# Kernel optimization log

Hardware: AMD Instinct MI355X
Metric: run time of the kernel (lower is better)

## Reference

```python
import jax, jax.numpy as jnp
import numpy as np

EMB = 1024
HEADS = 16
S = EMB // HEADS  # per-head dim


def setup_inputs() -> dict:
    key = jax.random.key(0)
    ks = jax.random.split(key, 6)
    x = jax.random.normal(ks[0], (4, 2048, EMB), dtype=jnp.float32)
    # torch nn.Linear(s, s, bias=False): weight [out, in], y = x @ W.T
    Wk = jax.random.normal(ks[1], (S, S), dtype=jnp.float32) * (1.0 / np.sqrt(S))
    Wq = jax.random.normal(ks[2], (S, S), dtype=jnp.float32) * (1.0 / np.sqrt(S))
    Wv = jax.random.normal(ks[3], (S, S), dtype=jnp.float32) * (1.0 / np.sqrt(S))
    # unifyHeads: Linear(heads*s, emb) with bias
    Wu = jax.random.normal(ks[4], (EMB, EMB), dtype=jnp.float32) * (1.0 / np.sqrt(EMB))
    bu = jax.random.normal(ks[5], (EMB,), dtype=jnp.float32) * 0.01
    return {"x": x, "Wk": Wk, "Wq": Wq, "Wv": Wv, "Wu": Wu, "bu": bu}


def reference(x, Wk, Wq, Wv, Wu, bu):
    b, t, e = x.shape
    h, s = HEADS, S
    x4 = x.reshape(b, t, h, s)
    # per-head narrow projections (y = x @ W.T)
    k = jnp.einsum('bths,os->bhto', x4, Wk)  # [b,h,t,s]
    q = jnp.einsum('bths,os->bhto', x4, Wq)
    v = jnp.einsum('bths,os->bhto', x4, Wv)
    scale = e ** 0.25
    q = q / scale
    k = k / scale
    dot = jnp.einsum('bhqs,bhks->bhqk', q, k)  # [b,h,t,t]
    attn = jax.nn.softmax(dot, axis=-1)
    out = jnp.einsum('bhqk,bhks->bhqs', attn, v)  # [b,h,t,s]
    out = out.transpose(0, 2, 1, 3).reshape(b, t, h * s)
    return out @ Wu.T + bu
```

## Files before the change

kernel.cpp:

```cpp
#include <hip/hip_runtime.h>
#include <hip/hip_bf16.h>

#define BB 4
#define TT 2048
#define HH 16
#define SS 64
#define EE 1024

typedef __attribute__((ext_vector_type(8))) short short8;
typedef __attribute__((ext_vector_type(4))) short short4v;
typedef __attribute__((ext_vector_type(4))) float float4v;
typedef unsigned long long ull;

__device__ inline short f2bf(float f) {
    union { __hip_bfloat16 h; short s; } u;
    u.h = __float2bfloat16(f);
    return u.s;
}

__device__ inline unsigned pack_bf(float lo, float hi) {
    return ((unsigned)(unsigned short)f2bf(hi) << 16) | (unsigned short)f2bf(lo);
}

__device__ inline unsigned pack_trunc(float lo, float hi) {
    unsigned a = __builtin_bit_cast(unsigned, lo);
    unsigned b = __builtin_bit_cast(unsigned, hi);
    return (b & 0xFFFF0000u) | (a >> 16);
}

__device__ inline float4v mfma16(short8 a, short8 b, float4v c) {
    return __builtin_amdgcn_mfma_f32_16x16x32_bf16(a, b, c, 0, 0, 0);
}

#define LDSP(p) ((__attribute__((address_space(3))) void*)(p))
#define GLBP(p) ((const __attribute__((address_space(1))) void*)(p))

__global__ __launch_bounds__(256) void k_qkv(
    const float* __restrict__ x, const float* __restrict__ Wk,
    const float* __restrict__ Wq, const float* __restrict__ Wv,
    short* __restrict__ qb, short* __restrict__ kb, short* __restrict__ vb)
{
    __shared__ __attribute__((aligned(16))) short lw[3][64][72];
    const int tid = threadIdx.x;
    const float sq = 0.21233045f;

    for (int i = 0; i < 12; i++) {
        int u = tid + 256 * i;
        int w = u >> 10;
        int rem = u & 1023;
        int row = rem >> 4;
        int col = (rem & 15) * 4;
        const float* Wp = (w == 0) ? Wk : ((w == 1) ? Wq : Wv);
        float4v f = *reinterpret_cast<const float4v*>(Wp + row * 64 + col);
        float sc = (w == 2) ? 1.0f : sq;
        short4v s4;
        s4.x = f2bf(f.x * sc); s4.y = f2bf(f.y * sc);
        s4.z = f2bf(f.z * sc); s4.w = f2bf(f.w * sc);
        *reinterpret_cast<short4v*>(&lw[w][row][col]) = s4;
    }
    __syncthreads();

    const int wave = tid >> 6, lane = tid & 63;
    const int quad = lane >> 4, m = lane & 15;
    const long r0 = (long)blockIdx.x * 64 + wave * 16;
    const int bt = (int)(r0 >> 4);
    const int b = bt >> 11, t = bt & 2047;

    const float* xrow = x + (r0 + m) * 64;
    short8 af[2];
    for (int ks = 0; ks < 2; ks++) {
        float4v f0 = *reinterpret_cast<const float4v*>(xrow + ks * 32 + quad * 8);
        float4v f1 = *reinterpret_cast<const float4v*>(xrow + ks * 32 + quad * 8 + 4);
        short8 a;
        a[0] = f2bf(f0.x); a[1] = f2bf(f0.y); a[2] = f2bf(f0.z); a[3] = f2bf(f0.w);
        a[4] = f2bf(f1.x); a[5] = f2bf(f1.y); a[6] = f2bf(f1.z); a[7] = f2bf(f1.w);
        af[ks] = a;
    }

    const long tb = ((long)(b * 16 + m) * 2048 + t) * 64;
    for (int w = 0; w < 3; w++) {
        short* dst = (w == 0) ? kb : ((w == 1) ? qb : vb);
        for (int c = 0; c < 4; c++) {
            float4v acc = {0.f, 0.f, 0.f, 0.f};
            for (int ks = 0; ks < 2; ks++) {
                short8 wf = *reinterpret_cast<const short8*>(&lw[w][c * 16 + m][ks * 32 + quad * 8]);
                acc = mfma16(wf, af[ks], acc);
            }
            unsigned lo = pack_bf(acc[0], acc[1]);
            unsigned hi = pack_bf(acc[2], acc[3]);
            ull wq = (ull)lo | ((ull)hi << 32);
            *reinterpret_cast<ull*>(dst + tb + c * 16 + quad * 4) = wq;
        }
    }
}

__global__ __launch_bounds__(256) void k_prep(
    const short* __restrict__ vb, short* __restrict__ vtb,
    const float* __restrict__ Wu, short* __restrict__ wub)
{
    __shared__ short lt[64][65];
    const int bid = blockIdx.x;
    const int tid = threadIdx.x;
    if (bid < 2048) {
        int bh = bid >> 5, tb = bid & 31;
        const short* src = vb + ((long)bh * 2048 + tb * 64) * 64;
        for (int i = 0; i < 2; i++) {
            int u = tid + 256 * i;
            int row = u >> 3, seg = u & 7;
            short8 d = *reinterpret_cast<const short8*>(src + row * 64 + seg * 8);
            for (int j = 0; j < 8; j++) lt[seg * 8 + j][row] = d[j];
        }
        __syncthreads();
        short* dst = vtb + (long)bh * 64 * 2048 + tb * 64;
        for (int i = 0; i < 2; i++) {
            int u = tid + 256 * i;
            int srow = u >> 3, seg = u & 7;
            short8 d;
            for (int j = 0; j < 8; j++) d[j] = lt[srow][seg * 8 + j];
            *reinterpret_cast<short8*>(dst + (long)srow * 2048 + seg * 8) = d;
        }
    } else {
        int cb = bid - 2048;
        long base = (long)cb * 4096;
        for (int i = 0; i < 4; i++) {
            long e = base + (long)tid * 4 + (long)i * 1024;
            float4v f = *reinterpret_cast<const float4v*>(Wu + e);
            short4v s;
            s.x = f2bf(f.x); s.y = f2bf(f.y); s.z = f2bf(f.z); s.w = f2bf(f.w);
            *reinterpret_cast<short4v*>(wub + e) = s;
        }
    }
}

__global__ __launch_bounds__(256, 2) void k_attn(
    const short* __restrict__ qb, const short* __restrict__ kb,
    const short* __restrict__ vtb, short* __restrict__ ob)
{
    __shared__ __attribute__((aligned(16))) short kt_s[2][4096];
    __shared__ __attribute__((aligned(16))) short vt_s[2][4096];

    const int tid = threadIdx.x;
    const int wave = tid >> 6, lane = tid & 63;
    const int quad = lane >> 4, m = lane & 15;
    const int qblk = blockIdx.x, bh = blockIdx.y;
    const int q0 = qblk * 256;
    const long qoff = (long)bh * 2048 * 64;

    const short* kbase = kb + qoff;
    const short* vtbase = vtb + (long)bh * 64 * 2048;

    short8 qf[4][2];
    for (int sub = 0; sub < 4; sub++) {
        const short* qrow = qb + qoff + (long)(q0 + wave * 64 + sub * 16 + m) * 64;
        qf[sub][0] = *reinterpret_cast<const short8*>(qrow + quad * 8);
        qf[sub][1] = *reinterpret_cast<const short8*>(qrow + 32 + quad * 8);
    }

    const short8 ones = (short8)((short)0x3F80);

    float4v oacc[4][4];
    float4v lacc[4];
    for (int s = 0; s < 4; s++) {
        lacc[s] = (float4v){0.f, 0.f, 0.f, 0.f};
        for (int c = 0; c < 4; c++) oacc[s][c] = (float4v){0.f, 0.f, 0.f, 0.f};
    }

    for (int i = 0; i < 2; i++) {
        int u = i * 256 + tid;
        int row = u >> 3;
        int cb = (u & 7) ^ (row & 7);
        const short* gp = kbase + (long)row * 64 + cb * 8;
        short* lp = &kt_s[0][(i * 256 + wave * 64) * 8];
        __builtin_amdgcn_global_load_lds(GLBP(gp), LDSP(lp), 16, 0, 0);
    }
    for (int i = 0; i < 2; i++) {
        int g = i * 256 + tid;
        int d = g >> 3, a = g & 7;
        union { short8 v; ull u[2]; } uv;
        uv.v = *reinterpret_cast<const short8*>(vtbase + (long)d * 2048 + a * 8);
        for (int h = 0; h < 2; h++) {
            int key0 = a * 8 + 4 * h;
            int c = key0 >> 4, qk = (key0 >> 2) & 3;
            int kk = (c >> 1) * 32 + qk * 8 + (c & 1) * 4;
            int idx = d * 64 + (((kk >> 3) ^ (d & 7)) * 8) + (kk & 7);
            *reinterpret_cast<ull*>(&vt_s[0][idx]) = uv.u[h];
        }
    }

    int p = 0;
    for (int kt = 0; kt < 32; kt++) {
        __syncthreads();

        const bool pref = (kt < 31);
        union { short8 v; ull u[2]; } vreg[2];
        if (pref) {
            for (int i = 0; i < 2; i++) {
                int u = i * 256 + tid;
                int row = u >> 3;
                int cb = (u & 7) ^ (row & 7);
                const short* gp = kbase + (long)((kt + 1) * 64 + row) * 64 + cb * 8;
                short* lp = &kt_s[p ^ 1][(i * 256 + wave * 64) * 8];
                __builtin_amdgcn_global_load_lds(GLBP(gp), LDSP(lp), 16, 0, 0);
            }
            for (int i = 0; i < 2; i++) {
                int g = i * 256 + tid;
                int d = g >> 3, a = g & 7;
                vreg[i].v = *reinterpret_cast<const short8*>(
                    vtbase + (long)d * 2048 + (kt + 1) * 64 + a * 8);
            }
        }

        short8 kf[4][2], vfr[4][2];
        for (int c = 0; c < 4; c++)
            for (int ks = 0; ks < 2; ks++)
                kf[c][ks] = *reinterpret_cast<const short8*>(
                    &kt_s[p][(c * 16 + m) * 64 + (((ks * 4 + quad) ^ (m & 7)) * 8)]);
        for (int c2 = 0; c2 < 4; c2++)
            for (int ks = 0; ks < 2; ks++)
                vfr[c2][ks] = *reinterpret_cast<const short8*>(
                    &vt_s[p][(c2 * 16 + m) * 64 + (((ks * 4 + quad) ^ (m & 7)) * 8)]);

        for (int sub = 0; sub < 4; sub++) {
            float4v st[4];
            for (int c = 0; c < 4; c++) {
                float4v z = {0.f, 0.f, 0.f, 0.f};
                z = mfma16(kf[c][0], qf[sub][0], z);
                z = mfma16(kf[c][1], qf[sub][1], z);
                st[c] = z;
            }
            __attribute__((aligned(16))) unsigned pp[8];
            for (int c = 0; c < 4; c++) {
                float e0 = __builtin_amdgcn_exp2f(st[c][0]);
                float e1 = __builtin_amdgcn_exp2f(st[c][1]);
                float e2 = __builtin_amdgcn_exp2f(st[c][2]);
                float e3 = __builtin_amdgcn_exp2f(st[c][3]);
                pp[c * 2]     = pack_trunc(e0, e1);
                pp[c * 2 + 1] = pack_trunc(e2, e3);
            }
            const short8* pf = reinterpret_cast<const short8*>(pp);
            lacc[sub] = mfma16(ones, pf[0], lacc[sub]);
            lacc[sub] = mfma16(ones, pf[1], lacc[sub]);
            for (int ks = 0; ks < 2; ks++)
                for (int c2 = 0; c2 < 4; c2++)
                    oacc[sub][c2] = mfma16(vfr[c2][ks], pf[ks], oacc[sub][c2]);
        }

        if (pref) {
            for (int i = 0; i < 2; i++) {
                int g = i * 256 + tid;
                int d = g >> 3, a = g & 7;
                for (int h = 0; h < 2; h++) {
                    int key0 = a * 8 + 4 * h;
                    int c = key0 >> 4, qk = (key0 >> 2) & 3;
                    int kk = (c >> 1) * 32 + qk * 8 + (c & 1) * 4;
                    int idx = d * 64 + (((kk >> 3) ^ (d & 7)) * 8) + (kk & 7);
                    *reinterpret_cast<ull*>(&vt_s[p ^ 1][idx]) = vreg[i].u[h];
                }
            }
        }
        p ^= 1;
    }

    const int b = bh >> 4, h = bh & 15;
    for (int sub = 0; sub < 4; sub++) {
        float li = 1.0f / lacc[sub][0];
        int t = q0 + wave * 64 + sub * 16 + m;
        long rowbase = (((long)(b * 2048 + t)) * 16 + h) * 64;
        for (int c2 = 0; c2 < 4; c2++) {
            unsigned w0 = pack_bf(oacc[sub][c2][0] * li, oacc[sub][c2][1] * li);
            unsigned w1 = pack_bf(oacc[sub][c2][2] * li, oacc[sub][c2][3] * li);
            ull wq = (ull)w0 | ((ull)w1 << 32);
            *reinterpret_cast<ull*>(ob + rowbase + c2 * 16 + quad * 4) = wq;
        }
    }
}

__global__ __launch_bounds__(256) void k_out(
    const short* __restrict__ ob, const short* __restrict__ wub,
    const float* __restrict__ bu, float* __restrict__ y)
{
    __shared__ __attribute__((aligned(16))) short a_s[8192];
    __shared__ __attribute__((aligned(16))) short b_s[8192];

    const int tid = threadIdx.x;
    const int wave = tid >> 6, lane = tid & 63;
    const int quad = lane >> 4, m = lane & 15;
    const int nb = blockIdx.x, mb = blockIdx.y;
    const long mbase = (long)mb * 128;
    const int nbase = nb * 128;
    const int wm = (wave & 1) * 64, wn = (wave >> 1) * 64;

    float4v acc[4][4];
    for (int i = 0; i < 4; i++)
        for (int j = 0; j < 4; j++) acc[i][j] = (float4v){0.f, 0.f, 0.f, 0.f};

    for (int kt = 0; kt < 16; kt++) {
        for (int i = 0; i < 4; i++) {
            int u = i * 256 + tid;
            int row = u >> 3;
            int c = (u & 7) ^ (row & 7);
            const short* gpA = ob + (mbase + row) * 1024 + kt * 64 + c * 8;
            const short* gpB = wub + (long)(nbase + row) * 1024 + kt * 64 + c * 8;
            short* lpA = a_s + (i * 256 + wave * 64) * 8;
            short* lpB = b_s + (i * 256 + wave * 64) * 8;
            __builtin_amdgcn_global_load_lds(GLBP(gpA), LDSP(lpA), 16, 0, 0);
            __builtin_amdgcn_global_load_lds(GLBP(gpB), LDSP(lpB), 16, 0, 0);
        }
        __syncthreads();
        for (int ks = 0; ks < 2; ks++) {
            short8 af[4], bf[4];
            for (int i = 0; i < 4; i++)
                af[i] = *reinterpret_cast<const short8*>(
                    a_s + (wm + i * 16 + m) * 64 + (((ks * 4 + quad) ^ (m & 7)) * 8));
            for (int j = 0; j < 4; j++)
                bf[j] = *reinterpret_cast<const short8*>(
                    b_s + (wn + j * 16 + m) * 64 + (((ks * 4 + quad) ^ (m & 7)) * 8));
            for (int i = 0; i < 4; i++)
                for (int j = 0; j < 4; j++)
                    acc[i][j] = mfma16(af[i], bf[j], acc[i][j]);
        }
        __syncthreads();
    }

    for (int j = 0; j < 4; j++) {
        int o = nbase + wn + j * 16 + m;
        float bias = bu[o];
        for (int i = 0; i < 4; i++) {
            for (int r = 0; r < 4; r++) {
                long row = mbase + wm + i * 16 + quad * 4 + r;
                y[row * 1024 + o] = acc[i][j][r] + bias;
            }
        }
    }
}

extern "C" void kernel_launch(void* const* d_in, const int* in_sizes, int n_in,
                              void* d_out, int out_size, void* d_ws, size_t ws_size,
                              hipStream_t stream)
{
    const float* x  = (const float*)d_in[0];
    const float* Wk = (const float*)d_in[1];
    const float* Wq = (const float*)d_in[2];
    const float* Wv = (const float*)d_in[3];
    const float* Wu = (const float*)d_in[4];
    const float* bu = (const float*)d_in[5];
    float* y = (float*)d_out;

    char* ws = (char*)d_ws;
    const size_t SEG = 16777216;
    short* qb  = (short*)(ws);
    short* kb  = (short*)(ws + 1 * SEG);
    short* vb  = (short*)(ws + 2 * SEG);
    short* vtb = (short*)(ws + 3 * SEG);
    short* ob  = (short*)(ws + 4 * SEG);
    short* wub = (short*)(ws + 5 * SEG);

    hipLaunchKernelGGL(k_qkv, dim3(2048), dim3(256), 0, stream, x, Wk, Wq, Wv, qb, kb, vb);
    hipLaunchKernelGGL(k_prep, dim3(2304), dim3(256), 0, stream, vb, vtb, Wu, wub);
    hipLaunchKernelGGL(k_attn, dim3(8, 64), dim3(256), 0, stream, qb, kb, vtb, ob);
    hipLaunchKernelGGL(k_out, dim3(8, 64), dim3(256), 0, stream, ob, wub, bu, y);
}
```

Before: 211.8 us.

## Batch QKV rows per block, VALU row sums in attention, double-buffer output GEMM

k_qkv now processes four 64-row groups per block, cutting the grid to 512 blocks so the LDS weight staging is amortised. In k_attn, the softmax row-sum now comes from VALU adds on the truncated exponentials plus a cross-lane shuffle reduction instead of extra MFMAs with a ones matrix, and all QK^T tiles are computed before the V fragments are loaded. k_out double-buffers its LDS tiles so the next K-slice loads overlap the MFMAs, at the cost of twice the shared memory. The risks are higher register pressure from st[4][4] and lower occupancy in k_out.

New measurement: 216.0 us. No clear change (+2.0%).

```diff
diff --git a/kernel.cpp b/kernel.cpp
--- a/kernel.cpp
+++ b/kernel.cpp
@@ -62,34 +62,37 @@
 
     const int wave = tid >> 6, lane = tid & 63;
     const int quad = lane >> 4, m = lane & 15;
-    const long r0 = (long)blockIdx.x * 64 + wave * 16;
-    const int bt = (int)(r0 >> 4);
-    const int b = bt >> 11, t = bt & 2047;
-
-    const float* xrow = x + (r0 + m) * 64;
-    short8 af[2];
-    for (int ks = 0; ks < 2; ks++) {
-        float4v f0 = *reinterpret_cast<const float4v*>(xrow + ks * 32 + quad * 8);
-        float4v f1 = *reinterpret_cast<const float4v*>(xrow + ks * 32 + quad * 8 + 4);
-        short8 a;
-        a[0] = f2bf(f0.x); a[1] = f2bf(f0.y); a[2] = f2bf(f0.z); a[3] = f2bf(f0.w);
-        a[4] = f2bf(f1.x); a[5] = f2bf(f1.y); a[6] = f2bf(f1.z); a[7] = f2bf(f1.w);
-        af[ks] = a;
-    }
-
-    const long tb = ((long)(b * 16 + m) * 2048 + t) * 64;
-    for (int w = 0; w < 3; w++) {
-        short* dst = (w == 0) ? kb : ((w == 1) ? qb : vb);
-        for (int c = 0; c < 4; c++) {
-            float4v acc = {0.f, 0.f, 0.f, 0.f};
-            for (int ks = 0; ks < 2; ks++) {
-                short8 wf = *reinterpret_cast<const short8*>(&lw[w][c * 16 + m][ks * 32 + quad * 8]);
-                acc = mfma16(wf, af[ks], acc);
-            }
-            unsigned lo = pack_bf(acc[0], acc[1]);
-            unsigned hi = pack_bf(acc[2], acc[3]);
-            ull wq = (ull)lo | ((ull)hi << 32);
-            *reinterpret_cast<ull*>(dst + tb + c * 16 + quad * 4) = wq;
+
+    for (int rg = 0; rg < 4; rg++) {
+        const long r0 = (long)blockIdx.x * 256 + rg * 64 + wave * 16;
+        const int bt = (int)(r0 >> 4);
+        const int b = bt >> 11, t = bt & 2047;
+
+        const float* xrow = x + (r0 + m) * 64;
+        short8 af[2];
+        for (int ks = 0; ks < 2; ks++) {
+            float4v f0 = *reinterpret_cast<const float4v*>(xrow + ks * 32 + quad * 8);
+            float4v f1 = *reinterpret_cast<const float4v*>(xrow + ks * 32 + quad * 8 + 4);
+            short8 a;
+            a[0] = f2bf(f0.x); a[1] = f2bf(f0.y); a[2] = f2bf(f0.z); a[3] = f2bf(f0.w);
+            a[4] = f2bf(f1.x); a[5] = f2bf(f1.y); a[6] = f2bf(f1.z); a[7] = f2bf(f1.w);
+            af[ks] = a;
+        }
+
+        const long tb = ((long)(b * 16 + m) * 2048 + t) * 64;
+        for (int w = 0; w < 3; w++) {
+            short* dst = (w == 0) ? kb : ((w == 1) ? qb : vb);
+            for (int c = 0; c < 4; c++) {
+                float4v acc = {0.f, 0.f, 0.f, 0.f};
+                for (int ks = 0; ks < 2; ks++) {
+                    short8 wf = *reinterpret_cast<const short8*>(&lw[w][c * 16 + m][ks * 32 + quad * 8]);
+                    acc = mfma16(wf, af[ks], acc);
+                }
+                unsigned lo = pack_bf(acc[0], acc[1]);
+                unsigned hi = pack_bf(acc[2], acc[3]);
+                ull wq = (ull)lo | ((ull)hi << 32);
+                *reinterpret_cast<ull*>(dst + tb + c * 16 + quad * 4) = wq;
+            }
         }
     }
 }
@@ -156,14 +159,10 @@
         qf[sub][1] = *reinterpret_cast<const short8*>(qrow + 32 + quad * 8);
     }
 
-    const short8 ones = (short8)((short)0x3F80);
-
+    float l[4] = {0.f, 0.f, 0.f, 0.f};
     float4v oacc[4][4];
-    float4v lacc[4];
-    for (int s = 0; s < 4; s++) {
-        lacc[s] = (float4v){0.f, 0.f, 0.f, 0.f};
+    for (int s = 0; s < 4; s++)
         for (int c = 0; c < 4; c++) oacc[s][c] = (float4v){0.f, 0.f, 0.f, 0.f};
-    }
 
     for (int i = 0; i < 2; i++) {
         int u = i * 256 + tid;
@@ -210,36 +209,44 @@
             }
         }
 
-        short8 kf[4][2], vfr[4][2];
+        short8 kf[4][2];
         for (int c = 0; c < 4; c++)
             for (int ks = 0; ks < 2; ks++)
                 kf[c][ks] = *reinterpret_cast<const short8*>(
                     &kt_s[p][(c * 16 + m) * 64 + (((ks * 4 + quad) ^ (m & 7)) * 8)]);
+
+        float4v st[4][4];
+        for (int sub = 0; sub < 4; sub++)
+            for (int c = 0; c < 4; c++) {
+                float4v z = {0.f, 0.f, 0.f, 0.f};
+                z = mfma16(kf[c][0], qf[sub][0], z);
+                st[sub][c] = mfma16(kf[c][1], qf[sub][1], z);
+            }
+
+        short8 vfr[4][2];
         for (int c2 = 0; c2 < 4; c2++)
             for (int ks = 0; ks < 2; ks++)
                 vfr[c2][ks] = *reinterpret_cast<const short8*>(
                     &vt_s[p][(c2 * 16 + m) * 64 + (((ks * 4 + quad) ^ (m & 7)) * 8)]);
 
         for (int sub = 0; sub < 4; sub++) {
-            float4v st[4];
-            for (int c = 0; c < 4; c++) {
-                float4v z = {0.f, 0.f, 0.f, 0.f};
-                z = mfma16(kf[c][0], qf[sub][0], z);
-                z = mfma16(kf[c][1], qf[sub][1], z);
-                st[c] = z;
-            }
             __attribute__((aligned(16))) unsigned pp[8];
             for (int c = 0; c < 4; c++) {
-                float e0 = __builtin_amdgcn_exp2f(st[c][0]);
-                float e1 = __builtin_amdgcn_exp2f(st[c][1]);
-                float e2 = __builtin_amdgcn_exp2f(st[c][2]);
-                float e3 = __builtin_amdgcn_exp2f(st[c][3]);
+                float e0 = __builtin_amdgcn_exp2f(st[sub][c][0]);
+                float e1 = __builtin_amdgcn_exp2f(st[sub][c][1]);
+                float e2 = __builtin_amdgcn_exp2f(st[sub][c][2]);
+                float e3 = __builtin_amdgcn_exp2f(st[sub][c][3]);
                 pp[c * 2]     = pack_trunc(e0, e1);
                 pp[c * 2 + 1] = pack_trunc(e2, e3);
             }
+            float ls = 0.f;
+            for (int i = 0; i < 8; i++) {
+                float flo = __builtin_bit_cast(float, pp[i] << 16);
+                float fhi = __builtin_bit_cast(float, pp[i] & 0xFFFF0000u);
+                ls += flo + fhi;
+            }
+            l[sub] += ls;
             const short8* pf = reinterpret_cast<const short8*>(pp);
-            lacc[sub] = mfma16(ones, pf[0], lacc[sub]);
-            lacc[sub] = mfma16(ones, pf[1], lacc[sub]);
             for (int ks = 0; ks < 2; ks++)
                 for (int c2 = 0; c2 < 4; c2++)
                     oacc[sub][c2] = mfma16(vfr[c2][ks], pf[ks], oacc[sub][c2]);
@@ -263,7 +270,10 @@
 
     const int b = bh >> 4, h = bh & 15;
     for (int sub = 0; sub < 4; sub++) {
-        float li = 1.0f / lacc[sub][0];
+        float lv = l[sub];
+        lv += __shfl_xor(lv, 16);
+        lv += __shfl_xor(lv, 32);
+        float li = 1.0f / lv;
         int t = q0 + wave * 64 + sub * 16 + m;
         long rowbase = (((long)(b * 2048 + t)) * 16 + h) * 64;
         for (int c2 = 0; c2 < 4; c2++) {
@@ -279,8 +289,8 @@
     const short* __restrict__ ob, const short* __restrict__ wub,
     const float* __restrict__ bu, float* __restrict__ y)
 {
-    __shared__ __attribute__((aligned(16))) short a_s[8192];
-    __shared__ __attribute__((aligned(16))) short b_s[8192];
+    __shared__ __attribute__((aligned(16))) short a_s[2][8192];
+    __shared__ __attribute__((aligned(16))) short b_s[2][8192];
 
     const int tid = threadIdx.x;
     const int wave = tid >> 6, lane = tid & 63;
@@ -294,32 +304,47 @@
     for (int i = 0; i < 4; i++)
         for (int j = 0; j < 4; j++) acc[i][j] = (float4v){0.f, 0.f, 0.f, 0.f};
 
+    for (int i = 0; i < 4; i++) {
+        int u = i * 256 + tid;
+        int row = u >> 3;
+        int c = (u & 7) ^ (row & 7);
+        const short* gpA = ob + (mbase + row) * 1024 + c * 8;
+        const short* gpB = wub + (long)(nbase + row) * 1024 + c * 8;
+        short* lpA = &a_s[0][(i * 256 + wave * 64) * 8];
+        short* lpB = &b_s[0][(i * 256 + wave * 64) * 8];
+        __builtin_amdgcn_global_load_lds(GLBP(gpA), LDSP(lpA), 16, 0, 0);
+        __builtin_amdgcn_global_load_lds(GLBP(gpB), LDSP(lpB), 16, 0, 0);
+    }
+
+    int p = 0;
     for (int kt = 0; kt < 16; kt++) {
-        for (int i = 0; i < 4; i++) {
-            int u = i * 256 + tid;
-            int row = u >> 3;
-            int c = (u & 7) ^ (row & 7);
-            const short* gpA = ob + (mbase + row) * 1024 + kt * 64 + c * 8;
-            const short* gpB = wub + (long)(nbase + row) * 1024 + kt * 64 + c * 8;
-            short* lpA = a_s + (i * 256 + wave * 64) * 8;
-            short* lpB = b_s + (i * 256 + wave * 64) * 8;
-            __builtin_amdgcn_global_load_lds(GLBP(gpA), LDSP(lpA), 16, 0, 0);
-            __builtin_amdgcn_global_load_lds(GLBP(gpB), LDSP(lpB), 16, 0, 0);
-        }
         __syncthreads();
+        if (kt < 15) {
+            for (int i = 0; i < 4; i++) {
+                int u = i * 256 + tid;
+                int row = u >> 3;
+                int c = (u & 7) ^ (row & 7);
+                const short* gpA = ob + (mbase + row) * 1024 + (kt + 1) * 64 + c * 8;
+                const short* gpB = wub + (long)(nbase + row) * 1024 + (kt + 1) * 64 + c * 8;
+                short* lpA = &a_s[p ^ 1][(i * 256 + wave * 64) * 8];
+                short* lpB = &b_s[p ^ 1][(i * 256 + wave * 64) * 8];
+                __builtin_amdgcn_global_load_lds(GLBP(gpA), LDSP(lpA), 16, 0, 0);
+                __builtin_amdgcn_global_load_lds(GLBP(gpB), LDSP(lpB), 16, 0, 0);
+            }
+        }
         for (int ks = 0; ks < 2; ks++) {
             short8 af[4], bf[4];
             for (int i = 0; i < 4; i++)
                 af[i] = *reinterpret_cast<const short8*>(
-                    a_s + (wm + i * 16 + m) * 64 + (((ks * 4 + quad) ^ (m & 7)) * 8));
+                    &a_s[p][(wm + i * 16 + m) * 64 + (((ks * 4 + quad) ^ (m & 7)) * 8)]);
             for (int j = 0; j < 4; j++)
                 bf[j] = *reinterpret_cast<const short8*>(
-                    b_s + (wn + j * 16 + m) * 64 + (((ks * 4 + quad) ^ (m & 7)) * 8));
+                    &b_s[p][(wn + j * 16 + m) * 64 + (((ks * 4 + quad) ^ (m & 7)) * 8)]);
             for (int i = 0; i < 4; i++)
                 for (int j = 0; j < 4; j++)
                     acc[i][j] = mfma16(af[i], bf[j], acc[i][j]);
         }
-        __syncthreads();
+        p ^= 1;
     }
 
     for (int j = 0; j < 4; j++) {
@@ -355,7 +380,7 @@
     short* ob  = (short*)(ws + 4 * SEG);
     short* wub = (short*)(ws + 5 * SEG);
 
-    hipLaunchKernelGGL(k_qkv, dim3(2048), dim3(256), 0, stream, x, Wk, Wq, Wv, qb, kb, vb);
+    hipLaunchKernelGGL(k_qkv, dim3(512), dim3(256), 0, stream, x, Wk, Wq, Wv, qb, kb, vb);
     hipLaunchKernelGGL(k_prep, dim3(2304), dim3(256), 0, stream, vb, vtb, Wu, wub);
     hipLaunchKernelGGL(k_attn, dim3(8, 64), dim3(256), 0, stream, qb, kb, vtb, ob);
     hipLaunchKernelGGL(k_out, dim3(8, 64), dim3(256), 0, stream, ob, wub, bu, y);
```
